# Optimization experiments

Measured on AMD Instinct MI355X. Metric: run time of the kernel, lower is better.

The kernel has to match this reference:

```python
import jax, jax.numpy as jnp
import numpy as np

TOP_K = 30
NUM_RBF = 16
MAXREL = 32


def _normalize(x, eps=1e-12):
    return x / jnp.maximum(jnp.linalg.norm(x, axis=-1, keepdims=True), eps)


def gather_edges(edges, idx):
    # edges [B,L,L,C], idx [B,L,K] -> [B,L,K,C]
    return jnp.take_along_axis(edges, idx[..., None], axis=2)


def gather_nodes(nodes, idx):
    # nodes [B,L,C], idx [B,L,K] -> [B,L,K,C]
    B, L, K = idx.shape
    flat = idx.reshape(B, L * K)
    g = jnp.take_along_axis(nodes, flat[:, :, None], axis=1)
    return g.reshape(B, L, K, nodes.shape[-1])


def _rbf(D):
    mu = jnp.linspace(2.0, 22.0, NUM_RBF)
    sigma = (22.0 - 2.0) / NUM_RBF
    return jnp.exp(-(((D[..., None] - mu) / sigma) ** 2))


def _get_rbf(A, B, E_idx):
    D = jnp.sqrt(jnp.sum((A[:, :, None, :] - B[:, None, :, :]) ** 2, -1) + 1e-6)
    Dn = gather_edges(D[..., None], E_idx)[..., 0]
    return _rbf(Dn)


def _dist(X, mask, eps=1e-6):
    mask2 = mask[:, None, :] * mask[:, :, None]
    dX = X[:, None, :, :] - X[:, :, None, :]
    D = mask2 * jnp.sqrt(jnp.sum(dX ** 2, -1) + eps)
    D_max = jnp.max(D, -1, keepdims=True)
    D_adjust = D + (1.0 - mask2) * D_max
    k = min(TOP_K, X.shape[1])
    neg_vals, E_idx = jax.lax.top_k(-D_adjust, k)  # smallest-k distances
    D_neighbors = -neg_vals
    mask_neighbors = gather_edges(mask2[..., None], E_idx)
    return D_neighbors, E_idx, mask_neighbors


def _quaternions(R):
    # R [B,L,K,3,3] -> Q [B,L,K,4]
    diag = jnp.diagonal(R, axis1=-2, axis2=-1)
    Rxx, Ryy, Rzz = diag[..., 0], diag[..., 1], diag[..., 2]
    magnitudes = 0.5 * jnp.sqrt(jnp.abs(1.0 + jnp.stack(
        [Rxx - Ryy - Rzz, -Rxx + Ryy - Rzz, -Rxx - Ryy + Rzz], -1)))
    signs = jnp.sign(jnp.stack([
        R[..., 2, 1] - R[..., 1, 2],
        R[..., 0, 2] - R[..., 2, 0],
        R[..., 1, 0] - R[..., 0, 1]], -1))
    xyz = signs * magnitudes
    w = jnp.sqrt(jax.nn.relu(1.0 + jnp.sum(diag, -1, keepdims=True))) / 2.0
    Q = jnp.concatenate((xyz, w), -1)
    return _normalize(Q)


def _orientations_coarse(X, E_idx, eps=1e-6):
    dX = X[:, 1:, :] - X[:, :-1, :]
    dX_norm = jnp.linalg.norm(dX, axis=-1)
    dX_mask = ((dX_norm > 3.6) & (dX_norm < 4.0)).astype(X.dtype)
    dX = dX * dX_mask[:, :, None]
    U = _normalize(dX)
    u_2, u_1, u_0 = U[:, :-2, :], U[:, 1:-1, :], U[:, 2:, :]
    n_2 = _normalize(jnp.cross(u_2, u_1))
    n_1 = _normalize(jnp.cross(u_1, u_0))
    cosA = jnp.clip(-(u_1 * u_0).sum(-1), -1 + eps, 1 - eps)
    A = jnp.arccos(cosA)
    cosD = jnp.clip((n_2 * n_1).sum(-1), -1 + eps, 1 - eps)
    Dang = jnp.sign((u_2 * n_1).sum(-1)) * jnp.arccos(cosD)
    AD = jnp.stack((jnp.cos(A), jnp.sin(A) * jnp.cos(Dang),
                    jnp.sin(A) * jnp.sin(Dang)), -1)
    AD = jnp.pad(AD, ((0, 0), (1, 2), (0, 0)))  # [B,L,3]
    o_1 = _normalize(u_2 - u_1)
    O = jnp.stack((o_1, n_2, jnp.cross(o_1, n_2)), -2)  # [B,L-3,3,3]
    O = O.reshape(O.shape[0], O.shape[1], 9)
    O = jnp.pad(O, ((0, 0), (1, 2), (0, 0)))  # [B,L,9]
    O_nb = gather_nodes(O, E_idx).reshape(E_idx.shape[0], E_idx.shape[1], E_idx.shape[2], 3, 3)
    X_nb = gather_nodes(X, E_idx)
    Om = O.reshape(O.shape[0], O.shape[1], 3, 3)
    dXn = X_nb - X[:, :, None, :]
    dU = _normalize(jnp.einsum('blij,blkj->blki', Om, dXn))
    R = jnp.einsum('blji,blkjm->blkim', Om, O_nb)  # O^T @ O_neighbors
    Q = _quaternions(R)
    return AD, jnp.concatenate((dU, Q), -1)  # [B,L,3], [B,L,K,7]


def _forward(Ca, mask, residue_idx, chain_labels, pos_W, pos_b, edge_W, ln_g, ln_b):
    D_neighbors, E_idx, mask_neighbors = _dist(Ca, mask)
    Ca_0 = jnp.pad(Ca[:, :-1, :], ((0, 0), (1, 0), (0, 0)))
    Ca_1 = Ca
    Ca_2 = jnp.pad(Ca[:, 1:, :], ((0, 0), (0, 1), (0, 0)))
    V, O_features = _orientations_coarse(Ca, E_idx)
    RBF_all = jnp.concatenate([
        _rbf(D_neighbors),
        _get_rbf(Ca_0, Ca_0, E_idx),
        _get_rbf(Ca_2, Ca_2, E_idx),
        _get_rbf(Ca_0, Ca_1, E_idx),
        _get_rbf(Ca_0, Ca_2, E_idx),
        _get_rbf(Ca_1, Ca_0, E_idx),
        _get_rbf(Ca_1, Ca_2, E_idx),
        _get_rbf(Ca_2, Ca_0, E_idx),
        _get_rbf(Ca_2, Ca_1, E_idx)], -1)  # [B,L,K,144]
    offset = residue_idx[:, :, None] - residue_idx[:, None, :]
    offset = gather_edges(offset[..., None], E_idx)[..., 0]
    d_chains = (chain_labels[:, :, None] - chain_labels[:, None, :] == 0).astype(jnp.int32)
    E_chains = gather_edges(d_chains[..., None], E_idx)[..., 0]
    d = jnp.clip(offset + MAXREL, 0, 2 * MAXREL) * E_chains + (1 - E_chains) * (2 * MAXREL + 1)
    d_onehot = jax.nn.one_hot(d, 2 * MAXREL + 2, dtype=pos_W.dtype)
    E_positional = d_onehot @ pos_W + pos_b
    E = jnp.concatenate((E_positional, RBF_all, O_features), -1)  # [B,L,K,167]
    E = E @ edge_W  # no bias
    mu = jnp.mean(E, -1, keepdims=True)
    var = jnp.var(E, -1, keepdims=True)
    E = (E - mu) / jnp.sqrt(var + 1e-5) * ln_g + ln_b
    return E, E_idx


def setup_inputs() -> dict:
    key = jax.random.key(0)
    k1, k2, k3 = jax.random.split(key, 3)
    B, L = 2, 4096
    Ca = jax.random.normal(k1, (B, L, 3), dtype=jnp.float32) * 10.0
    mask = jnp.ones((B, L), dtype=jnp.float32)
    residue_idx = jnp.arange(B * L, dtype=jnp.int32).reshape(B, L) % L
    chain_labels = jnp.zeros((B, L), dtype=jnp.int32)
    pos_W = jax.random.normal(k2, (2 * MAXREL + 2, 16), dtype=jnp.float32) * 0.1
    pos_b = jnp.zeros((16,), dtype=jnp.float32)
    edge_in = 16 + NUM_RBF * 9 + 7  # 167
    edge_W = jax.random.normal(k3, (edge_in, 128), dtype=jnp.float32) * 0.05
    ln_g = jnp.ones((128,), dtype=jnp.float32)
    ln_b = jnp.zeros((128,), dtype=jnp.float32)
    return {"Ca": Ca, "mask": mask, "residue_idx": residue_idx,
            "chain_labels": chain_labels, "pos_W": pos_W, "pos_b": pos_b,
            "edge_W": edge_W, "ln_g": ln_g, "ln_b": ln_b}


def reference(Ca, mask, residue_idx, chain_labels, pos_W, pos_b, edge_W, ln_g, ln_b):
    return _forward(Ca, mask, residue_idx, chain_labels, pos_W, pos_b, edge_W, ln_g, ln_b)
```

## Files before the change

kernel.cpp:

```cpp
#include <hip/hip_runtime.h>
#include <math.h>

constexpr int Lc   = 4096;
constexpr int Bc   = 2;
constexpr int KNB  = 30;
constexpr int NF   = 167;
constexpr int NC   = 128;
constexpr int KP   = 200;
constexpr int NKT  = 6;
constexpr int CAP  = 512;

typedef __attribute__((ext_vector_type(8))) short bf16x8;
typedef __attribute__((ext_vector_type(4))) float f32x4;

struct V3 { float x, y, z; };

__device__ __forceinline__ float sgnf(float v) {
    return (v > 0.f) ? 1.f : ((v < 0.f) ? -1.f : 0.f);
}
__device__ __forceinline__ unsigned long long umin64(unsigned long long a, unsigned long long b) {
    return a < b ? a : b;
}
__device__ __forceinline__ void splitbf(float v, unsigned short& h, unsigned short& l) {
    unsigned u = __float_as_uint(v);
    h = (unsigned short)(u >> 16);
    float fh = __uint_as_float((unsigned)h << 16);
    l = (unsigned short)(__float_as_uint(v - fh) >> 16);
}
__device__ __forceinline__ unsigned short bf16rne(float v) {
    unsigned u = __float_as_uint(v);
    return (unsigned short)((u + 0x7FFFu + ((u >> 16) & 1u)) >> 16);
}

__global__ void pack_kernel(const float* __restrict__ W,
                            unsigned short* __restrict__ Wh,
                            unsigned short* __restrict__ Wl) {
    int t = blockIdx.x * blockDim.x + threadIdx.x;
    if (t >= NKT * 8 * 64) return;
    int lane = t & 63, nt = (t >> 6) & 7, kt = t >> 9;
    int n = nt * 16 + (lane & 15);
    int kbase = kt * 32 + (lane >> 4) * 8;
    __align__(16) unsigned short h[8], l[8];
#pragma unroll
    for (int j = 0; j < 8; ++j) {
        int k = kbase + j;
        float v = (k < NF) ? W[(size_t)k * NC + n] : 0.f;
        splitbf(v, h[j], l[j]);
    }
    size_t o = (size_t)t * 8;
    *(bf16x8*)(Wh + o) = *(const bf16x8*)h;
    *(bf16x8*)(Wl + o) = *(const bf16x8*)l;
}

__global__ __launch_bounds__(256) void topk_kernel(
    const float* __restrict__ Ca, const float* __restrict__ mask,
    float* __restrict__ Dn, float* __restrict__ EidxF, int* __restrict__ EidxI) {
    const int row = blockIdx.x;
    const int b = row >> 12, i = row & (Lc - 1);
    const float* CaB = Ca + (size_t)b * Lc * 3;
    const float* mB  = mask + (size_t)b * Lc;
    const float xi = CaB[i * 3 + 0], yi = CaB[i * 3 + 1], zi = CaB[i * 3 + 2];
    const float mi = mB[i];

    __shared__ unsigned long long cand[CAP];
    __shared__ float redf[4];
    __shared__ int redi[2][4];
    __shared__ int candN;

    const int t = threadIdx.x, lane = t & 63, wid = t >> 6;
    if (t == 0) candN = 0;

    float dm[16], m2a[16];
    float lmax = -1e30f;
#pragma unroll
    for (int k = 0; k < 16; ++k) {
        int j = t + k * 256;
        float dx = CaB[j * 3 + 0] - xi;
        float dy = CaB[j * 3 + 1] - yi;
        float dz = CaB[j * 3 + 2] - zi;
        float d = sqrtf(dx * dx + dy * dy + dz * dz + 1e-6f);
        float m2 = mi * mB[j];
        float v = m2 * d;
        dm[k] = v; m2a[k] = m2;
        lmax = fmaxf(lmax, v);
    }
    for (int off = 32; off; off >>= 1) lmax = fmaxf(lmax, __shfl_xor(lmax, off));
    if (lane == 0) redf[wid] = lmax;
    __syncthreads();
    const float dmax = fmaxf(fmaxf(redf[0], redf[1]), fmaxf(redf[2], redf[3]));

#pragma unroll
    for (int k = 0; k < 16; ++k) dm[k] = dm[k] + (1.f - m2a[k]) * dmax;

    float T = dmax * 0.19435f;
    int c = 0;
    for (int iter = 0; iter < 32; ++iter) {
        int lc = 0;
#pragma unroll
        for (int k = 0; k < 16; ++k) lc += (dm[k] <= T) ? 1 : 0;
        for (int off = 32; off; off >>= 1) lc += __shfl_xor(lc, off);
        if (lane == 0) redi[iter & 1][wid] = lc;
        __syncthreads();
        c = redi[iter & 1][0] + redi[iter & 1][1] + redi[iter & 1][2] + redi[iter & 1][3];
        if (c >= KNB && c <= 64) break;
        if (iter >= 12 && c >= KNB && c <= CAP) break;
        if (c < KNB)
            T *= (c == 0) ? 1.7f
                          : fminf(1.7f, 1.05f * cbrtf((float)(KNB + 15) / (float)c));
        else
            T *= fmaxf(0.55f, 1.05f * cbrtf(45.f / (float)c));
    }

#pragma unroll
    for (int k = 0; k < 16; ++k) {
        if (dm[k] <= T) {
            int idx = atomicAdd(&candN, 1);
            if (idx < CAP)
                cand[idx] = ((unsigned long long)__float_as_uint(dm[k]) << 32) |
                            (unsigned)(t + k * 256);
        }
    }
    __syncthreads();

    if (wid == 0) {
        int C = candN; if (C > CAP) C = CAP;
        if (C <= 64) {
            unsigned long long key = (lane < C) ? cand[lane] : ~0ULL;
#pragma unroll
            for (int size = 2; size <= 64; size <<= 1) {
#pragma unroll
                for (int stride = size >> 1; stride; stride >>= 1) {
                    unsigned long long other = __shfl_xor(key, stride);
                    bool dirUp = ((lane & size) == 0);
                    bool takeMin = ((lane & stride) == 0) ? dirUp : !dirUp;
                    bool less = other < key;
                    unsigned long long mn = less ? other : key;
                    unsigned long long mx = less ? key : other;
                    key = takeMin ? mn : mx;
                }
            }
            if (lane < KNB) {
                int jw = (int)(key & 0xFFFFFFFFULL);
                EidxF[(size_t)row * KNB + lane] = (float)jw;
                EidxI[(size_t)row * KNB + lane] = jw;
                Dn[(size_t)row * KNB + lane] = __uint_as_float((unsigned)(key >> 32));
            }
        } else {
            unsigned long long r[CAP / 64];
#pragma unroll
            for (int q = 0; q < CAP / 64; ++q) {
                int idx = lane + q * 64;
                r[q] = (idx < C) ? cand[idx] : ~0ULL;
            }
            for (int p = 0; p < KNB; ++p) {
                unsigned long long mn = r[0];
#pragma unroll
                for (int q = 1; q < CAP / 64; ++q) mn = umin64(mn, r[q]);
                for (int off = 32; off; off >>= 1) mn = umin64(mn, __shfl_xor(mn, off));
                if (lane == 0) {
                    int jw = (int)(mn & 0xFFFFFFFFULL);
                    EidxF[(size_t)row * KNB + p] = (float)jw;
                    EidxI[(size_t)row * KNB + p] = jw;
                    Dn[(size_t)row * KNB + p] = __uint_as_float((unsigned)(mn >> 32));
                }
#pragma unroll
                for (int q = 0; q < CAP / 64; ++q) if (r[q] == mn) r[q] = ~0ULL;
            }
        }
    }
}

__device__ __forceinline__ V3 unit_seg(float dx, float dy, float dz) {
    float n = sqrtf(dx * dx + dy * dy + dz * dz);
    float m = (n > 3.6f && n < 4.0f) ? 1.f : 0.f;
    float nn = fmaxf(m * n, 1e-12f);
    V3 r; r.x = dx * m / nn; r.y = dy * m / nn; r.z = dz * m / nn;
    return r;
}

__global__ void orient_kernel(const float* __restrict__ Ca, float* __restrict__ O) {
    int idx = blockIdx.x * blockDim.x + threadIdx.x;
    if (idx >= Bc * Lc) return;
    int b = idx >> 12, l = idx & (Lc - 1);
    float* o = O + (size_t)idx * 9;
    if (l < 1 || l >= Lc - 2) {
#pragma unroll
        for (int q = 0; q < 9; ++q) o[q] = 0.f;
        return;
    }
    const float* C = Ca + ((size_t)b * Lc + (l - 1)) * 3;
    float ax = C[0], ay = C[1], az = C[2];
    float bx = C[3], by = C[4], bz = C[5];
    float cx = C[6], cy = C[7], cz = C[8];
    V3 u2 = unit_seg(bx - ax, by - ay, bz - az);
    V3 u1 = unit_seg(cx - bx, cy - by, cz - bz);
    float nx = u2.y * u1.z - u2.z * u1.y;
    float ny = u2.z * u1.x - u2.x * u1.z;
    float nz = u2.x * u1.y - u2.y * u1.x;
    float nn = fmaxf(sqrtf(nx * nx + ny * ny + nz * nz), 1e-12f);
    nx /= nn; ny /= nn; nz /= nn;
    float ox = u2.x - u1.x, oy = u2.y - u1.y, oz = u2.z - u1.z;
    float on = fmaxf(sqrtf(ox * ox + oy * oy + oz * oz), 1e-12f);
    ox /= on; oy /= on; oz /= on;
    float rx = oy * nz - oz * ny;
    float ry = oz * nx - ox * nz;
    float rz = ox * ny - oy * nx;
    o[0] = ox; o[1] = oy; o[2] = oz;
    o[3] = nx; o[4] = ny; o[5] = nz;
    o[6] = rx; o[7] = ry; o[8] = rz;
}

__global__ __launch_bounds__(256) void edge_kernel(
    const float* __restrict__ Ca, const int* __restrict__ ridx,
    const int* __restrict__ clab, const float* __restrict__ pos_W,
    const float* __restrict__ pos_b,
    const unsigned short* __restrict__ Wh, const unsigned short* __restrict__ Wl,
    const float* __restrict__ ln_g, const float* __restrict__ ln_b,
    const float* __restrict__ Dn, const int* __restrict__ EidxI,
    const float* __restrict__ Omat, float* __restrict__ outE) {
    const int row = blockIdx.x;
    const int b = row >> 12, i = row & (Lc - 1);
    const int tid = threadIdx.x, lane = tid & 63, w = tid >> 6;

    __shared__ __align__(16) unsigned short Fh[32][KP];
    __shared__ float Ssum[32][4];
    __shared__ float Ssq[32][4];
    __shared__ float2 Mstat[32];
    __shared__ int Ej[32];

    const float* CaB = Ca + (size_t)b * Lc * 3;

    for (int q = tid; q < 32 * 33; q += 256) {
        int r = q / 33, c = 167 + q % 33;
        Fh[r][c] = 0;
    }
    for (int q = tid; q < 2 * 167; q += 256) {
        int r = 30 + q / 167, c = q % 167;
        Fh[r][c] = 0;
    }
    if (tid < KNB) Ej[tid] = EidxI[(size_t)row * KNB + tid];
    __syncthreads();

    auto putF = [&](int e, int k, float v) { Fh[e][k] = bf16rne(v); };
    auto loadC = [&](int n) {
        V3 r;
        if (n >= 0 && n < Lc) { r.x = CaB[n*3]; r.y = CaB[n*3+1]; r.z = CaB[n*3+2]; }
        else { r.x = 0.f; r.y = 0.f; r.z = 0.f; }
        return r;
    };
    const int pa_t[10] = {0,0,0,2,0,0,1,1,2,2};
    const int pb_t[10] = {0,0,0,2,1,2,0,2,0,1};

    for (int task = tid; task < 330; task += 256) {
        int e = task % 30;
        int g = task / 30;
        int j = Ej[e];
        if (g == 0) {
            int off = ridx[(size_t)b * Lc + i] - ridx[(size_t)b * Lc + j];
            int ec = (clab[(size_t)b * Lc + i] == clab[(size_t)b * Lc + j]) ? 1 : 0;
            int d = ec ? min(max(off + 32, 0), 64) : 65;
#pragma unroll
            for (int c = 0; c < 16; ++c) putF(e, c, pos_W[d * 16 + c] + pos_b[c]);
        } else if (g < 10) {
            float D;
            if (g == 1) {
                D = Dn[(size_t)row * KNB + e];
            } else {
                V3 A = loadC(i - 1 + pa_t[g]);
                V3 B = loadC(j - 1 + pb_t[g]);
                float dx = A.x - B.x, dy = A.y - B.y, dz = A.z - B.z;
                D = sqrtf(dx * dx + dy * dy + dz * dz + 1e-6f);
            }
            int k0 = 16 * g;
#pragma unroll
            for (int m = 0; m < 16; ++m) {
                float mu = 2.f + (20.f / 15.f) * (float)m;
                float z = (D - mu) * (1.f / 1.25f);
                putF(e, k0 + m, __expf(-z * z));
            }
        } else {
            const float* Om = Omat + (size_t)row * 9;
            const float* On = Omat + ((size_t)b * Lc + j) * 9;
            V3 Ai = loadC(i), Bj = loadC(j);
            float dvx = Bj.x - Ai.x, dvy = Bj.y - Ai.y, dvz = Bj.z - Ai.z;
            float u0 = Om[0] * dvx + Om[1] * dvy + Om[2] * dvz;
            float u1 = Om[3] * dvx + Om[4] * dvy + Om[5] * dvz;
            float u2 = Om[6] * dvx + Om[7] * dvy + Om[8] * dvz;
            float un = fmaxf(sqrtf(u0 * u0 + u1 * u1 + u2 * u2), 1e-12f);
            putF(e, 160, u0 / un); putF(e, 161, u1 / un); putF(e, 162, u2 / un);
            float R[3][3];
#pragma unroll
            for (int a = 0; a < 3; ++a)
#pragma unroll
                for (int m = 0; m < 3; ++m)
                    R[a][m] = Om[0 * 3 + a] * On[0 * 3 + m] +
                              Om[1 * 3 + a] * On[1 * 3 + m] +
                              Om[2 * 3 + a] * On[2 * 3 + m];
            float Rxx = R[0][0], Ryy = R[1][1], Rzz = R[2][2];
            float m0 = 0.5f * sqrtf(fabsf(1.f + Rxx - Ryy - Rzz));
            float m1 = 0.5f * sqrtf(fabsf(1.f - Rxx + Ryy - Rzz));
            float m2 = 0.5f * sqrtf(fabsf(1.f - Rxx - Ryy + Rzz));
            float qx = sgnf(R[2][1] - R[1][2]) * m0;
            float qy = sgnf(R[0][2] - R[2][0]) * m1;
            float qz = sgnf(R[1][0] - R[0][1]) * m2;
            float qw = sqrtf(fmaxf(0.f, 1.f + Rxx + Ryy + Rzz)) * 0.5f;
            float qn = fmaxf(sqrtf(qx * qx + qy * qy + qz * qz + qw * qw), 1e-12f);
            putF(e, 163, qx / qn); putF(e, 164, qy / qn);
            putF(e, 165, qz / qn); putF(e, 166, qw / qn);
        }
    }
    __syncthreads();

    const int arow = lane & 15, agrp = lane >> 4;
    const int ng0 = w * 2;
    f32x4 acc[2][2];
#pragma unroll
    for (int m = 0; m < 2; ++m)
#pragma unroll
        for (int n = 0; n < 2; ++n) acc[m][n] = (f32x4){0.f, 0.f, 0.f, 0.f};

    const bf16x8* WhF = (const bf16x8*)Wh;
    const bf16x8* WlF = (const bf16x8*)Wl;

#pragma unroll
    for (int kt = 0; kt < NKT; ++kt) {
        const int kof = kt * 32 + agrp * 8;
        bf16x8 a0 = *(const bf16x8*)&Fh[arow][kof];
        bf16x8 a1 = *(const bf16x8*)&Fh[16 + arow][kof];
        bf16x8 b0h = WhF[(kt * 8 + ng0) * 64 + lane];
        bf16x8 b1h = WhF[(kt * 8 + ng0 + 1) * 64 + lane];
        bf16x8 b0l = WlF[(kt * 8 + ng0) * 64 + lane];
        bf16x8 b1l = WlF[(kt * 8 + ng0 + 1) * 64 + lane];

        acc[0][0] = __builtin_amdgcn_mfma_f32_16x16x32_bf16(a0, b0h, acc[0][0], 0, 0, 0);
        acc[0][0] = __builtin_amdgcn_mfma_f32_16x16x32_bf16(a0, b0l, acc[0][0], 0, 0, 0);
        acc[0][1] = __builtin_amdgcn_mfma_f32_16x16x32_bf16(a0, b1h, acc[0][1], 0, 0, 0);
        acc[0][1] = __builtin_amdgcn_mfma_f32_16x16x32_bf16(a0, b1l, acc[0][1], 0, 0, 0);
        acc[1][0] = __builtin_amdgcn_mfma_f32_16x16x32_bf16(a1, b0h, acc[1][0], 0, 0, 0);
        acc[1][0] = __builtin_amdgcn_mfma_f32_16x16x32_bf16(a1, b0l, acc[1][0], 0, 0, 0);
        acc[1][1] = __builtin_amdgcn_mfma_f32_16x16x32_bf16(a1, b1h, acc[1][1], 0, 0, 0);
        acc[1][1] = __builtin_amdgcn_mfma_f32_16x16x32_bf16(a1, b1l, acc[1][1], 0, 0, 0);
    }

    float ps[2][4], pq[2][4];
#pragma unroll
    for (int m = 0; m < 2; ++m)
#pragma unroll
        for (int r = 0; r < 4; ++r) {
            float v0 = acc[m][0][r], v1 = acc[m][1][r];
            ps[m][r] = v0 + v1;
            pq[m][r] = v0 * v0 + v1 * v1;
        }
#pragma unroll
    for (int off = 1; off < 16; off <<= 1) {
#pragma unroll
        for (int m = 0; m < 2; ++m)
#pragma unroll
            for (int r = 0; r < 4; ++r) {
                ps[m][r] += __shfl_xor(ps[m][r], off);
                pq[m][r] += __shfl_xor(pq[m][r], off);
            }
    }
    if (arow == 0) {
#pragma unroll
        for (int m = 0; m < 2; ++m)
#pragma unroll
            for (int r = 0; r < 4; ++r) {
                int me = m * 16 + agrp * 4 + r;
                Ssum[me][w] = ps[m][r];
                Ssq[me][w] = pq[m][r];
            }
    }
    __syncthreads();
    if (tid < 32) {
        float s = Ssum[tid][0] + Ssum[tid][1] + Ssum[tid][2] + Ssum[tid][3];
        float q = Ssq[tid][0] + Ssq[tid][1] + Ssq[tid][2] + Ssq[tid][3];
        float mean = s * (1.f / 128.f);
        float var = q * (1.f / 128.f) - mean * mean;
        Mstat[tid] = make_float2(mean, 1.f / sqrtf(var + 1e-5f));
    }
    __syncthreads();

    float gg[2], bb[2];
#pragma unroll
    for (int n = 0; n < 2; ++n) {
        int ce = (ng0 + n) * 16 + arow;
        gg[n] = ln_g[ce];
        bb[n] = ln_b[ce];
    }
#pragma unroll
    for (int m = 0; m < 2; ++m)
#pragma unroll
        for (int r = 0; r < 4; ++r) {
            int me = m * 16 + agrp * 4 + r;
            if (me >= KNB) continue;
            float2 st = Mstat[me];
            size_t base = ((size_t)row * KNB + me) * NC;
#pragma unroll
            for (int n = 0; n < 2; ++n) {
                int ce = (ng0 + n) * 16 + arow;
                outE[base + ce] = (acc[m][n][r] - st.x) * st.y * gg[n] + bb[n];
            }
        }
}

extern "C" void kernel_launch(void* const* d_in, const int* in_sizes, int n_in,
                              void* d_out, int out_size, void* d_ws, size_t ws_size,
                              hipStream_t stream) {
    const float* Ca     = (const float*)d_in[0];
    const float* mask   = (const float*)d_in[1];
    const int*   ridx   = (const int*)d_in[2];
    const int*   clab   = (const int*)d_in[3];
    const float* pos_W  = (const float*)d_in[4];
    const float* pos_b  = (const float*)d_in[5];
    const float* edge_W = (const float*)d_in[6];
    const float* ln_g   = (const float*)d_in[7];
    const float* ln_b   = (const float*)d_in[8];

    float* outE  = (float*)d_out;
    float* EidxF = outE + (size_t)Bc * Lc * KNB * NC;

    float* Dn    = (float*)d_ws;
    float* Omat  = Dn + (size_t)Bc * Lc * KNB;
    int*   EidxI = (int*)(Omat + (size_t)Bc * Lc * 9);
    unsigned short* Wh = (unsigned short*)(EidxI + (size_t)Bc * Lc * KNB);
    unsigned short* Wl = Wh + (size_t)NKT * 8 * 64 * 8;

    const int rows = Bc * Lc;
    pack_kernel<<<12, 256, 0, stream>>>(edge_W, Wh, Wl);
    topk_kernel<<<rows, 256, 0, stream>>>(Ca, mask, Dn, EidxF, EidxI);
    orient_kernel<<<(rows + 255) / 256, 256, 0, stream>>>(Ca, Omat);
    edge_kernel<<<rows, 256, 0, stream>>>(Ca, ridx, clab, pos_W, pos_b, Wh, Wl,
                                          ln_g, ln_b, Dn, EidxI, Omat, outE);
}
```

Measured before the change: 133.4 us.

## Fuse top-k neighbor selection into edge feature kernel

Merges the per-row top-k kernel into the edge featurization kernel, so the neighbor indices and distances stay in shared memory instead of going through global workspace. This removes one kernel launch and the Dn/EidxI global round trip. In exchange, shared memory and register use per block go up, which may lower occupancy, and the top-k phase no longer overlaps with other work.

```diff
diff --git a/kernel.cpp b/kernel.cpp
--- a/kernel.cpp
+++ b/kernel.cpp
@@ -50,124 +50,6 @@
     size_t o = (size_t)t * 8;
     *(bf16x8*)(Wh + o) = *(const bf16x8*)h;
     *(bf16x8*)(Wl + o) = *(const bf16x8*)l;
-}
-
-__global__ __launch_bounds__(256) void topk_kernel(
-    const float* __restrict__ Ca, const float* __restrict__ mask,
-    float* __restrict__ Dn, float* __restrict__ EidxF, int* __restrict__ EidxI) {
-    const int row = blockIdx.x;
-    const int b = row >> 12, i = row & (Lc - 1);
-    const float* CaB = Ca + (size_t)b * Lc * 3;
-    const float* mB  = mask + (size_t)b * Lc;
-    const float xi = CaB[i * 3 + 0], yi = CaB[i * 3 + 1], zi = CaB[i * 3 + 2];
-    const float mi = mB[i];
-
-    __shared__ unsigned long long cand[CAP];
-    __shared__ float redf[4];
-    __shared__ int redi[2][4];
-    __shared__ int candN;
-
-    const int t = threadIdx.x, lane = t & 63, wid = t >> 6;
-    if (t == 0) candN = 0;
-
-    float dm[16], m2a[16];
-    float lmax = -1e30f;
-#pragma unroll
-    for (int k = 0; k < 16; ++k) {
-        int j = t + k * 256;
-        float dx = CaB[j * 3 + 0] - xi;
-        float dy = CaB[j * 3 + 1] - yi;
-        float dz = CaB[j * 3 + 2] - zi;
-        float d = sqrtf(dx * dx + dy * dy + dz * dz + 1e-6f);
-        float m2 = mi * mB[j];
-        float v = m2 * d;
-        dm[k] = v; m2a[k] = m2;
-        lmax = fmaxf(lmax, v);
-    }
-    for (int off = 32; off; off >>= 1) lmax = fmaxf(lmax, __shfl_xor(lmax, off));
-    if (lane == 0) redf[wid] = lmax;
-    __syncthreads();
-    const float dmax = fmaxf(fmaxf(redf[0], redf[1]), fmaxf(redf[2], redf[3]));
-
-#pragma unroll
-    for (int k = 0; k < 16; ++k) dm[k] = dm[k] + (1.f - m2a[k]) * dmax;
-
-    float T = dmax * 0.19435f;
-    int c = 0;
-    for (int iter = 0; iter < 32; ++iter) {
-        int lc = 0;
-#pragma unroll
-        for (int k = 0; k < 16; ++k) lc += (dm[k] <= T) ? 1 : 0;
-        for (int off = 32; off; off >>= 1) lc += __shfl_xor(lc, off);
-        if (lane == 0) redi[iter & 1][wid] = lc;
-        __syncthreads();
-        c = redi[iter & 1][0] + redi[iter & 1][1] + redi[iter & 1][2] + redi[iter & 1][3];
-        if (c >= KNB && c <= 64) break;
-        if (iter >= 12 && c >= KNB && c <= CAP) break;
-        if (c < KNB)
-            T *= (c == 0) ? 1.7f
-                          : fminf(1.7f, 1.05f * cbrtf((float)(KNB + 15) / (float)c));
-        else
-            T *= fmaxf(0.55f, 1.05f * cbrtf(45.f / (float)c));
-    }
-
-#pragma unroll
-    for (int k = 0; k < 16; ++k) {
-        if (dm[k] <= T) {
-            int idx = atomicAdd(&candN, 1);
-            if (idx < CAP)
-                cand[idx] = ((unsigned long long)__float_as_uint(dm[k]) << 32) |
-                            (unsigned)(t + k * 256);
-        }
-    }
-    __syncthreads();
-
-    if (wid == 0) {
-        int C = candN; if (C > CAP) C = CAP;
-        if (C <= 64) {
-            unsigned long long key = (lane < C) ? cand[lane] : ~0ULL;
-#pragma unroll
-            for (int size = 2; size <= 64; size <<= 1) {
-#pragma unroll
-                for (int stride = size >> 1; stride; stride >>= 1) {
-                    unsigned long long other = __shfl_xor(key, stride);
-                    bool dirUp = ((lane & size) == 0);
-                    bool takeMin = ((lane & stride) == 0) ? dirUp : !dirUp;
-                    bool less = other < key;
-                    unsigned long long mn = less ? other : key;
-                    unsigned long long mx = less ? key : other;
-                    key = takeMin ? mn : mx;
-                }
-            }
-            if (lane < KNB) {
-                int jw = (int)(key & 0xFFFFFFFFULL);
-                EidxF[(size_t)row * KNB + lane] = (float)jw;
-                EidxI[(size_t)row * KNB + lane] = jw;
-                Dn[(size_t)row * KNB + lane] = __uint_as_float((unsigned)(key >> 32));
-            }
-        } else {
-            unsigned long long r[CAP / 64];
-#pragma unroll
-            for (int q = 0; q < CAP / 64; ++q) {
-                int idx = lane + q * 64;
-                r[q] = (idx < C) ? cand[idx] : ~0ULL;
-            }
-            for (int p = 0; p < KNB; ++p) {
-                unsigned long long mn = r[0];
-#pragma unroll
-                for (int q = 1; q < CAP / 64; ++q) mn = umin64(mn, r[q]);
-                for (int off = 32; off; off >>= 1) mn = umin64(mn, __shfl_xor(mn, off));
-                if (lane == 0) {
-                    int jw = (int)(mn & 0xFFFFFFFFULL);
-                    EidxF[(size_t)row * KNB + p] = (float)jw;
-                    EidxI[(size_t)row * KNB + p] = jw;
-                    Dn[(size_t)row * KNB + p] = __uint_as_float((unsigned)(mn >> 32));
-                }
-#pragma unroll
-                for (int q = 0; q < CAP / 64; ++q) if (r[q] == mn) r[q] = ~0ULL;
-            }
-        }
-    }
 }
 
 __device__ __forceinline__ V3 unit_seg(float dx, float dy, float dz) {
@@ -210,25 +92,32 @@
     o[6] = rx; o[7] = ry; o[8] = rz;
 }
 
-__global__ __launch_bounds__(256) void edge_kernel(
-    const float* __restrict__ Ca, const int* __restrict__ ridx,
-    const int* __restrict__ clab, const float* __restrict__ pos_W,
-    const float* __restrict__ pos_b,
+__global__ __launch_bounds__(256) void fused_kernel(
+    const float* __restrict__ Ca, const float* __restrict__ mask,
+    const int* __restrict__ ridx, const int* __restrict__ clab,
+    const float* __restrict__ pos_W, const float* __restrict__ pos_b,
     const unsigned short* __restrict__ Wh, const unsigned short* __restrict__ Wl,
     const float* __restrict__ ln_g, const float* __restrict__ ln_b,
-    const float* __restrict__ Dn, const int* __restrict__ EidxI,
-    const float* __restrict__ Omat, float* __restrict__ outE) {
+    const float* __restrict__ Omat,
+    float* __restrict__ outE, float* __restrict__ EidxF) {
     const int row = blockIdx.x;
     const int b = row >> 12, i = row & (Lc - 1);
     const int tid = threadIdx.x, lane = tid & 63, w = tid >> 6;
 
     __shared__ __align__(16) unsigned short Fh[32][KP];
+    __shared__ unsigned long long cand[CAP];
+    __shared__ float redf[4];
+    __shared__ int redi[2][4];
+    __shared__ int candN;
     __shared__ float Ssum[32][4];
     __shared__ float Ssq[32][4];
     __shared__ float2 Mstat[32];
     __shared__ int Ej[32];
+    __shared__ float DnS[32];
 
     const float* CaB = Ca + (size_t)b * Lc * 3;
+    const float* mB  = mask + (size_t)b * Lc;
+    if (tid == 0) candN = 0;
 
     for (int q = tid; q < 32 * 33; q += 256) {
         int r = q / 33, c = 167 + q % 33;
@@ -238,7 +127,108 @@
         int r = 30 + q / 167, c = q % 167;
         Fh[r][c] = 0;
     }
-    if (tid < KNB) Ej[tid] = EidxI[(size_t)row * KNB + tid];
+
+    const float xi = CaB[i * 3 + 0], yi = CaB[i * 3 + 1], zi = CaB[i * 3 + 2];
+    const float mi = mB[i];
+
+    float dm[16], m2a[16];
+    float lmax = -1e30f;
+#pragma unroll
+    for (int k = 0; k < 16; ++k) {
+        int j = tid + k * 256;
+        float dx = CaB[j * 3 + 0] - xi;
+        float dy = CaB[j * 3 + 1] - yi;
+        float dz = CaB[j * 3 + 2] - zi;
+        float d = sqrtf(dx * dx + dy * dy + dz * dz + 1e-6f);
+        float m2 = mi * mB[j];
+        float v = m2 * d;
+        dm[k] = v; m2a[k] = m2;
+        lmax = fmaxf(lmax, v);
+    }
+    for (int off = 32; off; off >>= 1) lmax = fmaxf(lmax, __shfl_xor(lmax, off));
+    if (lane == 0) redf[w] = lmax;
+    __syncthreads();
+    const float dmax = fmaxf(fmaxf(redf[0], redf[1]), fmaxf(redf[2], redf[3]));
+
+#pragma unroll
+    for (int k = 0; k < 16; ++k) dm[k] = dm[k] + (1.f - m2a[k]) * dmax;
+
+    float T = dmax * 0.19435f;
+    int c = 0;
+    for (int iter = 0; iter < 32; ++iter) {
+        int lc = 0;
+#pragma unroll
+        for (int k = 0; k < 16; ++k) lc += (dm[k] <= T) ? 1 : 0;
+        for (int off = 32; off; off >>= 1) lc += __shfl_xor(lc, off);
+        if (lane == 0) redi[iter & 1][w] = lc;
+        __syncthreads();
+        c = redi[iter & 1][0] + redi[iter & 1][1] + redi[iter & 1][2] + redi[iter & 1][3];
+        if (c >= KNB && c <= 64) break;
+        if (iter >= 12 && c >= KNB && c <= CAP) break;
+        if (c < KNB)
+            T *= (c == 0) ? 1.7f
+                          : fminf(1.7f, 1.05f * cbrtf((float)(KNB + 15) / (float)c));
+        else
+            T *= fmaxf(0.55f, 1.05f * cbrtf(45.f / (float)c));
+    }
+
+#pragma unroll
+    for (int k = 0; k < 16; ++k) {
+        if (dm[k] <= T) {
+            int idx = atomicAdd(&candN, 1);
+            if (idx < CAP)
+                cand[idx] = ((unsigned long long)__float_as_uint(dm[k]) << 32) |
+                            (unsigned)(tid + k * 256);
+        }
+    }
+    __syncthreads();
+
+    if (w == 0) {
+        int C = candN; if (C > CAP) C = CAP;
+        if (C <= 64) {
+            unsigned long long key = (lane < C) ? cand[lane] : ~0ULL;
+#pragma unroll
+            for (int size = 2; size <= 64; size <<= 1) {
+#pragma unroll
+                for (int stride = size >> 1; stride; stride >>= 1) {
+                    unsigned long long other = __shfl_xor(key, stride);
+                    bool dirUp = ((lane & size) == 0);
+                    bool takeMin = ((lane & stride) == 0) ? dirUp : !dirUp;
+                    bool less = other < key;
+                    unsigned long long mn = less ? other : key;
+                    unsigned long long mx = less ? key : other;
+                    key = takeMin ? mn : mx;
+                }
+            }
+            if (lane < KNB) {
+                int jw = (int)(key & 0xFFFFFFFFULL);
+                EidxF[(size_t)row * KNB + lane] = (float)jw;
+                Ej[lane] = jw;
+                DnS[lane] = __uint_as_float((unsigned)(key >> 32));
+            }
+        } else {
+            unsigned long long r[CAP / 64];
+#pragma unroll
+            for (int q = 0; q < CAP / 64; ++q) {
+                int idx = lane + q * 64;
+                r[q] = (idx < C) ? cand[idx] : ~0ULL;
+            }
+            for (int p = 0; p < KNB; ++p) {
+                unsigned long long mn = r[0];
+#pragma unroll
+                for (int q = 1; q < CAP / 64; ++q) mn = umin64(mn, r[q]);
+                for (int off = 32; off; off >>= 1) mn = umin64(mn, __shfl_xor(mn, off));
+                if (lane == 0) {
+                    int jw = (int)(mn & 0xFFFFFFFFULL);
+                    EidxF[(size_t)row * KNB + p] = (float)jw;
+                    Ej[p] = jw;
+                    DnS[p] = __uint_as_float((unsigned)(mn >> 32));
+                }
+#pragma unroll
+                for (int q = 0; q < CAP / 64; ++q) if (r[q] == mn) r[q] = ~0ULL;
+            }
+        }
+    }
     __syncthreads();
 
     auto putF = [&](int e, int k, float v) { Fh[e][k] = bf16rne(v); };
@@ -260,11 +250,11 @@
             int ec = (clab[(size_t)b * Lc + i] == clab[(size_t)b * Lc + j]) ? 1 : 0;
             int d = ec ? min(max(off + 32, 0), 64) : 65;
 #pragma unroll
-            for (int c = 0; c < 16; ++c) putF(e, c, pos_W[d * 16 + c] + pos_b[c]);
+            for (int cc = 0; cc < 16; ++cc) putF(e, cc, pos_W[d * 16 + cc] + pos_b[cc]);
         } else if (g < 10) {
             float D;
             if (g == 1) {
-                D = Dn[(size_t)row * KNB + e];
+                D = DnS[e];
             } else {
                 V3 A = loadC(i - 1 + pa_t[g]);
                 V3 B = loadC(j - 1 + pb_t[g]);
@@ -420,16 +410,13 @@
     float* outE  = (float*)d_out;
     float* EidxF = outE + (size_t)Bc * Lc * KNB * NC;
 
-    float* Dn    = (float*)d_ws;
-    float* Omat  = Dn + (size_t)Bc * Lc * KNB;
-    int*   EidxI = (int*)(Omat + (size_t)Bc * Lc * 9);
-    unsigned short* Wh = (unsigned short*)(EidxI + (size_t)Bc * Lc * KNB);
+    float* Omat  = (float*)d_ws;
+    unsigned short* Wh = (unsigned short*)(Omat + (size_t)Bc * Lc * 9);
     unsigned short* Wl = Wh + (size_t)NKT * 8 * 64 * 8;
 
     const int rows = Bc * Lc;
     pack_kernel<<<12, 256, 0, stream>>>(edge_W, Wh, Wl);
-    topk_kernel<<<rows, 256, 0, stream>>>(Ca, mask, Dn, EidxF, EidxI);
     orient_kernel<<<(rows + 255) / 256, 256, 0, stream>>>(Ca, Omat);
-    edge_kernel<<<rows, 256, 0, stream>>>(Ca, ridx, clab, pos_W, pos_b, Wh, Wl,
-                                          ln_g, ln_b, Dn, EidxI, Omat, outE);
-}
+    fused_kernel<<<rows, 256, 0, stream>>>(Ca, mask, ridx, clab, pos_W, pos_b,
+                                           Wh, Wl, ln_g, ln_b, Omat, outE, EidxF);
+}
```

Measured after the change: 137.5 us. +3.1%, slower.
